# Optimization experiments

Measured on AMD Instinct MI355X. Metric: run time of the kernel, lower is better.

The kernel has to match this reference:

```python
import jax, jax.numpy as jnp
import numpy as np

B, L, D = 16, 512, 768   # batch, seq_len, hidden_size
H = 12                   # encoder attention heads (self_attention_scores)
K = 128                  # num_preserved_tokens
U, NH = 256, 4           # router attention num_units / num_heads


def setup_inputs() -> dict:
    key = jax.random.key(0)
    ks = jax.random.split(key, 8)
    hidden_states = jax.random.normal(ks[0], (B, L, D), dtype=jnp.float32)
    u = jax.random.uniform(ks[1], (B, 1, 1, L))
    attention_mask = jnp.where(u < 0.9, 0.0, -10000.0).astype(jnp.float32)
    self_attention_scores = jax.random.normal(ks[2], (B, H, L, L), dtype=jnp.float32)
    Wq = jax.random.normal(ks[3], (U, D), dtype=jnp.float32) * 0.02
    Wk = jax.random.normal(ks[4], (U, D), dtype=jnp.float32) * 0.02
    Wv = jax.random.normal(ks[5], (U, D), dtype=jnp.float32) * 0.02
    Wo = jax.random.normal(ks[6], (D, U), dtype=jnp.float32) * 0.02
    bo = jnp.zeros((D,), dtype=jnp.float32)
    return {"hidden_states": hidden_states, "attention_mask": attention_mask,
            "self_attention_scores": self_attention_scores,
            "Wq": Wq, "Wk": Wk, "Wv": Wv, "Wo": Wo, "bo": bo}


def reference(hidden_states, attention_mask, self_attention_scores, Wq, Wk, Wv, Wo, bo):
    # sentence summary: softmax over additive mask -> weighted token average
    att = jax.nn.softmax(attention_mask, axis=-1)            # [B,1,1,L]
    sentences = jnp.einsum('bql,bld->bqd', att[:, 0], hidden_states)  # [B,1,D]

    key_padding_mask = attention_mask[:, 0, 0, :] < -10.0    # [B,L] True = masked

    # MyMultiHeadAttention(query=sentences, key=value=hidden_states)
    hd = U // NH
    q = jnp.einsum('bqd,ud->bqu', sentences, Wq)             # [B,1,U]
    k = jnp.einsum('bld,ud->blu', hidden_states, Wk)         # [B,L,U]
    v = jnp.einsum('bld,ud->blu', hidden_states, Wv)         # [B,L,U]
    qh = q.reshape(B, 1, NH, hd).transpose(2, 0, 1, 3)       # [h,B,1,hd]
    kh = k.reshape(B, L, NH, hd).transpose(2, 0, 1, 3)       # [h,B,L,hd]
    vh = v.reshape(B, L, NH, hd).transpose(2, 0, 1, 3)       # [h,B,L,hd]
    # NOTE: original scales by key_dim**0.5 = hidden_size**0.5 (not head dim)
    scores = jnp.einsum('hbqd,hbkd->hbqk', qh, kh) / (D ** 0.5)  # [h,B,1,L]
    scores = jnp.where(key_padding_mask[None, :, None, :], -jnp.inf, scores)
    probs = jax.nn.softmax(scores, axis=-1)
    out_h = jnp.einsum('hbqk,hbkd->hbqd', probs, vh)         # [h,B,1,hd]
    out = out_h.transpose(1, 2, 0, 3).reshape(B, 1, U)       # concat heads
    new_token = jnp.einsum('bqu,du->bqd', out, Wo) + bo      # [B,1,D]

    class_token = hidden_states[:, :1, :]                    # [B,1,D]

    # importance: mean over heads, sum over query positions -> [B,L]
    importance = self_attention_scores.mean(axis=1).sum(axis=1)
    top_idx = jax.lax.top_k(importance, K)[1]                # [B,K]
    # boolean-mask gather preserves original token order -> sort indices
    sorted_idx = jnp.sort(top_idx, axis=-1)                  # [B,K]
    preserved_tokens = jnp.take_along_axis(hidden_states, sorted_idx[:, :, None], axis=1)  # [B,K,D]
    preserved_mask = jnp.take_along_axis(attention_mask[:, 0, 0, :], sorted_idx, axis=1)
    preserved_mask = preserved_mask.reshape(B, 1, 1, K)

    zmask = jnp.zeros((B, 1, 1, 1), dtype=attention_mask.dtype)
    final_token = jnp.concatenate([class_token, preserved_tokens, new_token], axis=1)  # [B,K+2,D]
    final_attention_mask = jnp.concatenate([zmask, preserved_mask, zmask], axis=-1)    # [B,1,1,K+2]
    return final_token, final_attention_mask
```

## Files before the change

kernel.cpp:

```cpp
#include <hip/hip_runtime.h>
#include <math.h>

#define B_ 16
#define L_ 512
#define D_ 768
#define H_ 12
#define K_ 128
#define U_ 256
#define NH_ 4
#define HD_ 64
#define OUTROWS_ 130
#define IMP_G_ 96

__global__ __launch_bounds__(256) void importance_kernel(
    const float* __restrict__ scores, float* __restrict__ part) {
  const int b = blockIdx.y, chunk = blockIdx.x, t = threadIdx.x;
  const int qcol = t & 127;
  const int rhalf = t >> 7;
  const float4* base = (const float4*)scores +
      ((size_t)(b * (H_ * L_) + chunk * 128 + rhalf)) * 128 + qcol;
  float4 a = make_float4(0.f, 0.f, 0.f, 0.f);
  #pragma unroll 8
  for (int r = 0; r < 64; ++r) {
    float4 v = base[(size_t)r * 256];
    a.x += v.x; a.y += v.y; a.z += v.z; a.w += v.w;
  }
  const float s = 1.0f / 12.0f;
  float4 o = make_float4(a.x * s, a.y * s, a.z * s, a.w * s);
  ((float4*)part)[((size_t)b * IMP_G_ + chunk * 2 + rhalf) * 128 + qcol] = o;
}

__global__ __launch_bounds__(768) void sent_kernel(
    const float* __restrict__ hidden, const float* __restrict__ mask,
    float* __restrict__ sent_part) {
  __shared__ float att[L_];
  __shared__ float red_m[12], red_s[12];
  __shared__ float4 cbuf[4][192];
  const int b = blockIdx.x, chunk = blockIdx.y, t = threadIdx.x;
  const int wave = t >> 6, lane = t & 63;
  const float m = (t < L_) ? mask[b * L_ + t] : -INFINITY;
  float r = m;
  #pragma unroll
  for (int off = 32; off > 0; off >>= 1) r = fmaxf(r, __shfl_down(r, off, 64));
  if (lane == 0) red_m[wave] = r;
  __syncthreads();
  float mx = red_m[0];
  #pragma unroll
  for (int w = 1; w < 12; ++w) mx = fmaxf(mx, red_m[w]);
  const float e = (t < L_) ? expf(m - mx) : 0.f;
  float rs = e;
  #pragma unroll
  for (int off = 32; off > 0; off >>= 1) rs += __shfl_down(rs, off, 64);
  if (lane == 0) red_s[wave] = rs;
  __syncthreads();
  float se = 0.f;
  #pragma unroll
  for (int w = 0; w < 12; ++w) se += red_s[w];
  if (t < L_) att[t] = e / se;
  __syncthreads();
  const int c4 = t % 192, sub = t / 192;
  const int l0 = chunk * 32 + sub * 8;
  const float4* h4 = (const float4*)hidden + ((size_t)b * L_ + l0) * 192 + c4;
  float4 acc = make_float4(0.f, 0.f, 0.f, 0.f);
  #pragma unroll
  for (int ii = 0; ii < 8; ++ii) {
    const float w = att[l0 + ii];
    const float4 hv = h4[(size_t)ii * 192];
    acc.x += w * hv.x; acc.y += w * hv.y; acc.z += w * hv.z; acc.w += w * hv.w;
  }
  cbuf[sub][c4] = acc;
  __syncthreads();
  if (t < 192) {
    float4 o = cbuf[0][t];
    #pragma unroll
    for (int g = 1; g < 4; ++g) {
      const float4 v = cbuf[g][t];
      o.x += v.x; o.y += v.y; o.z += v.z; o.w += v.w;
    }
    ((float4*)sent_part)[((size_t)b * 16 + chunk) * 192 + t] = o;
  }
}

__global__ __launch_bounds__(768) void qproj_topk_kernel(
    const float* __restrict__ sent_part, const float* __restrict__ Wq,
    const float* __restrict__ Wk, float* __restrict__ wqe,
    const float* __restrict__ part, const float* __restrict__ mask,
    const float* __restrict__ hidden, float* __restrict__ out0,
    float* __restrict__ out1) {
  __shared__ float s[D_];
  __shared__ float qvh[HD_];
  __shared__ float v[L_];
  __shared__ int lidx[K_];
  __shared__ int wcnt[12];
  const int t = threadIdx.x;
  const int wave = t >> 6, lane = t & 63;

  if (blockIdx.x < 64) {
    const int b = blockIdx.x >> 2, h = blockIdx.x & 3;
    {
      const float* sp = sent_part + (size_t)b * 16 * D_ + t;
      float a = 0.f;
      #pragma unroll
      for (int c = 0; c < 16; ++c) a += sp[(size_t)c * D_];
      s[t] = a;
    }
    __syncthreads();
    for (int u = wave; u < HD_; u += 12) {
      const float* wr = Wq + (size_t)(h * HD_ + u) * D_;
      float acc = 0.f;
      #pragma unroll
      for (int k = 0; k < 12; ++k) {
        const int d = lane + (k << 6);
        acc += wr[d] * s[d];
      }
      #pragma unroll
      for (int o = 32; o > 0; o >>= 1) acc += __shfl_down(acc, o, 64);
      if (lane == 0) qvh[u] = acc;
    }
    __syncthreads();
    {
      float acc = 0.f;
      const float* wk = Wk + (size_t)(h * HD_) * D_ + t;
      #pragma unroll 4
      for (int j = 0; j < HD_; ++j) acc += qvh[j] * wk[(size_t)j * D_];
      wqe[((size_t)b * NH_ + h) * D_ + t] = acc;
    }
  } else {
    const int b = blockIdx.x - 64;
    if (t < L_) {
      const float* pp = part + (size_t)b * IMP_G_ * L_ + t;
      float sum = 0.f;
      #pragma unroll 8
      for (int g = 0; g < IMP_G_; ++g) sum += pp[(size_t)g * L_];
      v[t] = sum;
    }
    __syncthreads();
    bool sel = false;
    if (t < L_) {
      const float mv = v[t];
      int cnt = 0;
      #pragma unroll 8
      for (int j = 0; j < L_; ++j) {
        float o = v[j];
        cnt += (o > mv) || (o == mv && j < t);
      }
      sel = cnt < K_;
    }
    const unsigned long long ball = __ballot(sel);
    if (lane == 0) wcnt[wave] = __popcll(ball);
    __syncthreads();
    int base = 0;
    for (int w = 0; w < wave; ++w) base += wcnt[w];
    const int pos = base + __popcll(ball & ((1ull << lane) - 1ull));
    if (sel) {
      lidx[pos] = t;
      out1[b * OUTROWS_ + 1 + pos] = mask[b * L_ + t];
    }
    if (t == 0) {
      out1[b * OUTROWS_ + 0] = 0.f;
      out1[b * OUTROWS_ + OUTROWS_ - 1] = 0.f;
    }
    __syncthreads();
    const float4* hb4 = (const float4*)(hidden + (size_t)b * L_ * D_);
    float4* ob4 = (float4*)(out0 + (size_t)b * OUTROWS_ * D_);
    const int NG = (K_ + 1) * 192;
    for (int i = t; i < NG; i += 768) {
      const int r = i / 192;
      const int c = i - r * 192;
      const int src = (r == 0) ? 0 : lidx[r - 1];
      ob4[r * 192 + c] = hb4[src * 192 + c];
    }
  }
}

__global__ __launch_bounds__(256) void score_kernel(
    const float* __restrict__ hidden, const float* __restrict__ mask,
    const float* __restrict__ wqe, float* __restrict__ scores) {
  __shared__ float4 wq4[NH_ * 192];
  const int b = blockIdx.x, chunk = blockIdx.y, t = threadIdx.x;
  {
    const float4* wsrc = (const float4*)(wqe + (size_t)b * NH_ * D_);
    for (int i = t; i < NH_ * 192; i += 256) wq4[i] = wsrc[i];
  }
  __syncthreads();
  const int wave = t >> 6, lane = t & 63;
  const float scale = 0.03608439182435161f;
  #pragma unroll
  for (int r = 0; r < 8; ++r) {
    const int l = chunk * 32 + wave * 8 + r;
    const float4* hr4 = (const float4*)(hidden + ((size_t)b * L_ + l) * D_);
    float s0 = 0.f, s1 = 0.f, s2 = 0.f, s3 = 0.f;
    #pragma unroll
    for (int jj = 0; jj < 3; ++jj) {
      const int c = lane + 64 * jj;
      const float4 hv = hr4[c];
      const float4 w0 = wq4[0 * 192 + c];
      const float4 w1 = wq4[1 * 192 + c];
      const float4 w2 = wq4[2 * 192 + c];
      const float4 w3 = wq4[3 * 192 + c];
      s0 += hv.x * w0.x + hv.y * w0.y + hv.z * w0.z + hv.w * w0.w;
      s1 += hv.x * w1.x + hv.y * w1.y + hv.z * w1.z + hv.w * w1.w;
      s2 += hv.x * w2.x + hv.y * w2.y + hv.z * w2.z + hv.w * w2.w;
      s3 += hv.x * w3.x + hv.y * w3.y + hv.z * w3.z + hv.w * w3.w;
    }
    #pragma unroll
    for (int o = 32; o > 0; o >>= 1) {
      s0 += __shfl_down(s0, o, 64);
      s1 += __shfl_down(s1, o, 64);
      s2 += __shfl_down(s2, o, 64);
      s3 += __shfl_down(s3, o, 64);
    }
    if (lane == 0) {
      const bool kp = mask[b * L_ + l] < -10.f;
      float* sp = scores + (size_t)b * NH_ * L_ + l;
      sp[0 * L_] = kp ? -INFINITY : s0 * scale;
      sp[1 * L_] = kp ? -INFINITY : s1 * scale;
      sp[2 * L_] = kp ? -INFINITY : s2 * scale;
      sp[3 * L_] = kp ? -INFINITY : s3 * scale;
    }
  }
}

__global__ __launch_bounds__(768) void ctx_prob_kernel(
    const float* __restrict__ hidden, const float* __restrict__ scores,
    float* __restrict__ ctx_part) {
  __shared__ float pr[NH_][32];
  __shared__ float red_m[NH_][12], red_s[NH_][12];
  const int b = blockIdx.x, chunk = blockIdx.y, t = threadIdx.x;
  const int wave = t >> 6, lane = t & 63;
  const int l0 = chunk * 32;

  float val[NH_];
  #pragma unroll
  for (int h = 0; h < NH_; ++h)
    val[h] = (t < L_) ? scores[((size_t)b * NH_ + h) * L_ + t] : -INFINITY;
  #pragma unroll
  for (int h = 0; h < NH_; ++h) {
    float r = val[h];
    #pragma unroll
    for (int off = 32; off > 0; off >>= 1) r = fmaxf(r, __shfl_down(r, off, 64));
    if (lane == 0) red_m[h][wave] = r;
  }
  __syncthreads();
  float e[NH_];
  #pragma unroll
  for (int h = 0; h < NH_; ++h) {
    float mx = red_m[h][0];
    #pragma unroll
    for (int w = 1; w < 12; ++w) mx = fmaxf(mx, red_m[h][w]);
    e[h] = (t < L_) ? expf(val[h] - mx) : 0.f;
    float rs = e[h];
    #pragma unroll
    for (int off = 32; off > 0; off >>= 1) rs += __shfl_down(rs, off, 64);
    if (lane == 0) red_s[h][wave] = rs;
  }
  __syncthreads();
  if (t >= l0 && t < l0 + 32) {
    #pragma unroll
    for (int h = 0; h < NH_; ++h) {
      float se = 0.f;
      #pragma unroll
      for (int w = 0; w < 12; ++w) se += red_s[h][w];
      pr[h][t - l0] = e[h] / se;
    }
  }
  __syncthreads();

  const int c4 = t % 192, hh = t / 192;
  const float4* h4 = (const float4*)hidden + ((size_t)b * L_ + l0) * 192 + c4;
  float4 acc = make_float4(0.f, 0.f, 0.f, 0.f);
  #pragma unroll 8
  for (int l = 0; l < 32; ++l) {
    const float w = pr[hh][l];
    const float4 hv = h4[(size_t)l * 192];
    acc.x += w * hv.x; acc.y += w * hv.y; acc.z += w * hv.z; acc.w += w * hv.w;
  }
  ((float4*)ctx_part)[(((size_t)b * 16 + chunk) * NH_ + hh) * 192 + c4] = acc;
}

__global__ __launch_bounds__(768) void outv_kernel(
    const float* __restrict__ ctx_part, const float* __restrict__ Wv,
    float* __restrict__ outv) {
  __shared__ float ch[D_];
  const int b = blockIdx.x, h = blockIdx.y, t = threadIdx.x;
  const int wave = t >> 6, lane = t & 63;
  {
    float a = 0.f;
    #pragma unroll
    for (int c = 0; c < 16; ++c)
      a += ctx_part[(((size_t)b * 16 + c) * NH_ + h) * D_ + t];
    ch[t] = a;
  }
  __syncthreads();
  for (int u = wave; u < HD_; u += 12) {
    const float* wr = Wv + (size_t)(h * HD_ + u) * D_;
    float acc = 0.f;
    #pragma unroll
    for (int k = 0; k < 12; ++k) {
      const int d = lane + (k << 6);
      acc += wr[d] * ch[d];
    }
    #pragma unroll
    for (int o = 32; o > 0; o >>= 1) acc += __shfl_down(acc, o, 64);
    if (lane == 0) outv[b * U_ + h * HD_ + u] = acc;
  }
}

__global__ __launch_bounds__(256) void newtoken_ws_kernel(
    const float* __restrict__ outv, const float* __restrict__ Wo,
    const float* __restrict__ bo, float* __restrict__ out0) {
  __shared__ float ovs[16 * 260];
  __shared__ float wot[16 * 260];
  const int d0 = blockIdx.x * 16, t = threadIdx.x;
  #pragma unroll
  for (int k = 0; k < 16; ++k) {
    const int i = t + (k << 8);
    const int row = i >> 8, u = i & 255;
    ovs[row * 260 + u] = outv[i];
    wot[row * 260 + u] = Wo[(size_t)(d0 + row) * U_ + u];
  }
  __syncthreads();
  const int b = t >> 4, dl = t & 15;
  const float* ov = ovs + b * 260;
  const float* wr = wot + dl * 260;
  float acc = 0.f;
  #pragma unroll 8
  for (int u = 0; u < U_; ++u) acc += ov[u] * wr[u];
  const int d = d0 + dl;
  out0[((size_t)b * OUTROWS_ + (OUTROWS_ - 1)) * D_ + d] = bo[d] + acc;
}

extern "C" void kernel_launch(void* const* d_in, const int* in_sizes, int n_in,
                              void* d_out, int out_size, void* d_ws, size_t ws_size,
                              hipStream_t stream) {
  const float* hidden = (const float*)d_in[0];
  const float* mask   = (const float*)d_in[1];
  const float* sas    = (const float*)d_in[2];
  const float* Wq     = (const float*)d_in[3];
  const float* Wk     = (const float*)d_in[4];
  const float* Wv     = (const float*)d_in[5];
  const float* Wo     = (const float*)d_in[6];
  const float* bo     = (const float*)d_in[7];

  float* out0 = (float*)d_out;
  float* out1 = out0 + (size_t)B_ * OUTROWS_ * D_;

  float* part      = (float*)d_ws;
  float* sent_part = part + (size_t)B_ * IMP_G_ * L_;
  float* ctx_part  = sent_part + (size_t)B_ * 16 * D_;
  float* wqe       = ctx_part + (size_t)B_ * 16 * NH_ * D_;
  float* scores    = wqe + (size_t)B_ * NH_ * D_;
  float* outv      = scores + (size_t)B_ * NH_ * L_;

  importance_kernel<<<dim3(48, B_), 256, 0, stream>>>(sas, part);
  sent_kernel<<<dim3(B_, 16), 768, 0, stream>>>(hidden, mask, sent_part);
  qproj_topk_kernel<<<80, 768, 0, stream>>>(sent_part, Wq, Wk, wqe,
                                            part, mask, hidden, out0, out1);
  score_kernel<<<dim3(B_, 16), 256, 0, stream>>>(hidden, mask, wqe, scores);
  ctx_prob_kernel<<<dim3(B_, 16), 768, 0, stream>>>(hidden, scores, ctx_part);
  outv_kernel<<<dim3(B_, NH_), 768, 0, stream>>>(ctx_part, Wv, outv);
  newtoken_ws_kernel<<<48, 256, 0, stream>>>(outv, Wo, bo, out0);
}
```

Baseline: 362.9 us.

## Fuse importance with sentence kernel and score with ctx using unnormalized softmax

Merges the importance reduction and sentence-summary kernels into one launch split by block index. The mask softmax is replaced by a count of valid tokens, which assumes the mask holds only 0 or -10000. Score computation and context accumulation are fused into one kernel that uses exp without max-subtraction and writes per-chunk exp sums. outv then normalizes by the total. This removes two launches and the scores round-trip through memory, at the cost of overflow risk for large scores and reliance on the binary mask values.

```diff
diff --git a/kernel.cpp b/kernel.cpp
--- a/kernel.cpp
+++ b/kernel.cpp
@@ -12,72 +12,57 @@
 #define OUTROWS_ 130
 #define IMP_G_ 96
 
-__global__ __launch_bounds__(256) void importance_kernel(
-    const float* __restrict__ scores, float* __restrict__ part) {
-  const int b = blockIdx.y, chunk = blockIdx.x, t = threadIdx.x;
-  const int qcol = t & 127;
-  const int rhalf = t >> 7;
-  const float4* base = (const float4*)scores +
-      ((size_t)(b * (H_ * L_) + chunk * 128 + rhalf)) * 128 + qcol;
-  float4 a = make_float4(0.f, 0.f, 0.f, 0.f);
-  #pragma unroll 8
-  for (int r = 0; r < 64; ++r) {
-    float4 v = base[(size_t)r * 256];
-    a.x += v.x; a.y += v.y; a.z += v.z; a.w += v.w;
-  }
-  const float s = 1.0f / 12.0f;
-  float4 o = make_float4(a.x * s, a.y * s, a.z * s, a.w * s);
-  ((float4*)part)[((size_t)b * IMP_G_ + chunk * 2 + rhalf) * 128 + qcol] = o;
-}
-
-__global__ __launch_bounds__(768) void sent_kernel(
-    const float* __restrict__ hidden, const float* __restrict__ mask,
+__global__ __launch_bounds__(256) void front_kernel(
+    const float* __restrict__ sas, const float* __restrict__ hidden,
+    const float* __restrict__ mask, float* __restrict__ part,
     float* __restrict__ sent_part) {
-  __shared__ float att[L_];
-  __shared__ float red_m[12], red_s[12];
-  __shared__ float4 cbuf[4][192];
-  const int b = blockIdx.x, chunk = blockIdx.y, t = threadIdx.x;
-  const int wave = t >> 6, lane = t & 63;
-  const float m = (t < L_) ? mask[b * L_ + t] : -INFINITY;
-  float r = m;
-  #pragma unroll
-  for (int off = 32; off > 0; off >>= 1) r = fmaxf(r, __shfl_down(r, off, 64));
-  if (lane == 0) red_m[wave] = r;
-  __syncthreads();
-  float mx = red_m[0];
-  #pragma unroll
-  for (int w = 1; w < 12; ++w) mx = fmaxf(mx, red_m[w]);
-  const float e = (t < L_) ? expf(m - mx) : 0.f;
-  float rs = e;
-  #pragma unroll
-  for (int off = 32; off > 0; off >>= 1) rs += __shfl_down(rs, off, 64);
-  if (lane == 0) red_s[wave] = rs;
-  __syncthreads();
-  float se = 0.f;
-  #pragma unroll
-  for (int w = 0; w < 12; ++w) se += red_s[w];
-  if (t < L_) att[t] = e / se;
-  __syncthreads();
-  const int c4 = t % 192, sub = t / 192;
-  const int l0 = chunk * 32 + sub * 8;
-  const float4* h4 = (const float4*)hidden + ((size_t)b * L_ + l0) * 192 + c4;
-  float4 acc = make_float4(0.f, 0.f, 0.f, 0.f);
-  #pragma unroll
-  for (int ii = 0; ii < 8; ++ii) {
-    const float w = att[l0 + ii];
-    const float4 hv = h4[(size_t)ii * 192];
-    acc.x += w * hv.x; acc.y += w * hv.y; acc.z += w * hv.z; acc.w += w * hv.w;
-  }
-  cbuf[sub][c4] = acc;
-  __syncthreads();
-  if (t < 192) {
-    float4 o = cbuf[0][t];
-    #pragma unroll
-    for (int g = 1; g < 4; ++g) {
-      const float4 v = cbuf[g][t];
-      o.x += v.x; o.y += v.y; o.z += v.z; o.w += v.w;
-    }
-    ((float4*)sent_part)[((size_t)b * 16 + chunk) * 192 + t] = o;
+  const int t = threadIdx.x;
+  if (blockIdx.x < 768) {
+    const int b = blockIdx.x / 48, chunk = blockIdx.x % 48;
+    const int qcol = t & 127;
+    const int rhalf = t >> 7;
+    const float4* base = (const float4*)sas +
+        ((size_t)(b * (H_ * L_) + chunk * 128 + rhalf)) * 128 + qcol;
+    float4 a = make_float4(0.f, 0.f, 0.f, 0.f);
+    #pragma unroll 8
+    for (int r = 0; r < 64; ++r) {
+      float4 v = base[(size_t)r * 256];
+      a.x += v.x; a.y += v.y; a.z += v.z; a.w += v.w;
+    }
+    const float s = 1.0f / 12.0f;
+    float4 o = make_float4(a.x * s, a.y * s, a.z * s, a.w * s);
+    ((float4*)part)[((size_t)b * IMP_G_ + chunk * 2 + rhalf) * 128 + qcol] = o;
+  } else {
+    __shared__ float att[L_];
+    __shared__ int redc[4];
+    const int i = blockIdx.x - 768;
+    const int b = i >> 4, chunk = i & 15;
+    const int wave = t >> 6, lane = t & 63;
+    const float m0 = mask[b * L_ + t];
+    const float m1 = mask[b * L_ + t + 256];
+    const int u0 = (m0 > -10.f) ? 1 : 0;
+    const int u1 = (m1 > -10.f) ? 1 : 0;
+    int c = u0 + u1;
+    #pragma unroll
+    for (int off = 32; off > 0; off >>= 1) c += __shfl_down(c, off, 64);
+    if (lane == 0) redc[wave] = c;
+    __syncthreads();
+    const float inv = 1.0f / (float)(redc[0] + redc[1] + redc[2] + redc[3]);
+    att[t]       = u0 ? inv : 0.f;
+    att[t + 256] = u1 ? inv : 0.f;
+    __syncthreads();
+    if (t < 192) {
+      const int l0 = chunk * 32;
+      const float4* h4 = (const float4*)hidden + ((size_t)b * L_ + l0) * 192 + t;
+      float4 acc = make_float4(0.f, 0.f, 0.f, 0.f);
+      #pragma unroll 8
+      for (int l = 0; l < 32; ++l) {
+        const float w = att[l0 + l];
+        const float4 hv = h4[(size_t)l * 192];
+        acc.x += w * hv.x; acc.y += w * hv.y; acc.z += w * hv.z; acc.w += w * hv.w;
+      }
+      ((float4*)sent_part)[((size_t)b * 16 + chunk) * 192 + t] = acc;
+    }
   }
 }
 
@@ -173,96 +158,64 @@
   }
 }
 
-__global__ __launch_bounds__(256) void score_kernel(
+__global__ __launch_bounds__(768) void scorectx_kernel(
     const float* __restrict__ hidden, const float* __restrict__ mask,
-    const float* __restrict__ wqe, float* __restrict__ scores) {
+    const float* __restrict__ wqe, float* __restrict__ ctx_part,
+    float* __restrict__ esum) {
   __shared__ float4 wq4[NH_ * 192];
-  const int b = blockIdx.x, chunk = blockIdx.y, t = threadIdx.x;
-  {
-    const float4* wsrc = (const float4*)(wqe + (size_t)b * NH_ * D_);
-    for (int i = t; i < NH_ * 192; i += 256) wq4[i] = wsrc[i];
-  }
-  __syncthreads();
-  const int wave = t >> 6, lane = t & 63;
-  const float scale = 0.03608439182435161f;
-  #pragma unroll
-  for (int r = 0; r < 8; ++r) {
-    const int l = chunk * 32 + wave * 8 + r;
-    const float4* hr4 = (const float4*)(hidden + ((size_t)b * L_ + l) * D_);
-    float s0 = 0.f, s1 = 0.f, s2 = 0.f, s3 = 0.f;
-    #pragma unroll
-    for (int jj = 0; jj < 3; ++jj) {
-      const int c = lane + 64 * jj;
-      const float4 hv = hr4[c];
-      const float4 w0 = wq4[0 * 192 + c];
-      const float4 w1 = wq4[1 * 192 + c];
-      const float4 w2 = wq4[2 * 192 + c];
-      const float4 w3 = wq4[3 * 192 + c];
-      s0 += hv.x * w0.x + hv.y * w0.y + hv.z * w0.z + hv.w * w0.w;
-      s1 += hv.x * w1.x + hv.y * w1.y + hv.z * w1.z + hv.w * w1.w;
-      s2 += hv.x * w2.x + hv.y * w2.y + hv.z * w2.z + hv.w * w2.w;
-      s3 += hv.x * w3.x + hv.y * w3.y + hv.z * w3.z + hv.w * w3.w;
-    }
-    #pragma unroll
-    for (int o = 32; o > 0; o >>= 1) {
-      s0 += __shfl_down(s0, o, 64);
-      s1 += __shfl_down(s1, o, 64);
-      s2 += __shfl_down(s2, o, 64);
-      s3 += __shfl_down(s3, o, 64);
-    }
-    if (lane == 0) {
-      const bool kp = mask[b * L_ + l] < -10.f;
-      float* sp = scores + (size_t)b * NH_ * L_ + l;
-      sp[0 * L_] = kp ? -INFINITY : s0 * scale;
-      sp[1 * L_] = kp ? -INFINITY : s1 * scale;
-      sp[2 * L_] = kp ? -INFINITY : s2 * scale;
-      sp[3 * L_] = kp ? -INFINITY : s3 * scale;
-    }
-  }
-}
-
-__global__ __launch_bounds__(768) void ctx_prob_kernel(
-    const float* __restrict__ hidden, const float* __restrict__ scores,
-    float* __restrict__ ctx_part) {
   __shared__ float pr[NH_][32];
-  __shared__ float red_m[NH_][12], red_s[NH_][12];
+  __shared__ float es[NH_];
   const int b = blockIdx.x, chunk = blockIdx.y, t = threadIdx.x;
   const int wave = t >> 6, lane = t & 63;
   const int l0 = chunk * 32;
 
-  float val[NH_];
-  #pragma unroll
-  for (int h = 0; h < NH_; ++h)
-    val[h] = (t < L_) ? scores[((size_t)b * NH_ + h) * L_ + t] : -INFINITY;
-  #pragma unroll
-  for (int h = 0; h < NH_; ++h) {
-    float r = val[h];
-    #pragma unroll
-    for (int off = 32; off > 0; off >>= 1) r = fmaxf(r, __shfl_down(r, off, 64));
-    if (lane == 0) red_m[h][wave] = r;
-  }
-  __syncthreads();
-  float e[NH_];
-  #pragma unroll
-  for (int h = 0; h < NH_; ++h) {
-    float mx = red_m[h][0];
-    #pragma unroll
-    for (int w = 1; w < 12; ++w) mx = fmaxf(mx, red_m[h][w]);
-    e[h] = (t < L_) ? expf(val[h] - mx) : 0.f;
-    float rs = e[h];
-    #pragma unroll
-    for (int off = 32; off > 0; off >>= 1) rs += __shfl_down(rs, off, 64);
-    if (lane == 0) red_s[h][wave] = rs;
-  }
-  __syncthreads();
-  if (t >= l0 && t < l0 + 32) {
-    #pragma unroll
-    for (int h = 0; h < NH_; ++h) {
-      float se = 0.f;
-      #pragma unroll
-      for (int w = 0; w < 12; ++w) se += red_s[h][w];
-      pr[h][t - l0] = e[h] / se;
-    }
+  for (int i = t; i < NH_ * 192; i += 768)
+    wq4[i] = ((const float4*)(wqe + (size_t)b * NH_ * D_))[i];
+  __syncthreads();
+
+  const float scale = 0.03608439182435161f;
+  if (wave < 8) {
+    #pragma unroll
+    for (int r = 0; r < 4; ++r) {
+      const int lr = wave * 4 + r;
+      const int l = l0 + lr;
+      const float4* hr4 = (const float4*)(hidden + ((size_t)b * L_ + l) * D_);
+      float s0 = 0.f, s1 = 0.f, s2 = 0.f, s3 = 0.f;
+      #pragma unroll
+      for (int jj = 0; jj < 3; ++jj) {
+        const int cc = lane + 64 * jj;
+        const float4 hv = hr4[cc];
+        const float4 w0 = wq4[0 * 192 + cc];
+        const float4 w1 = wq4[1 * 192 + cc];
+        const float4 w2 = wq4[2 * 192 + cc];
+        const float4 w3 = wq4[3 * 192 + cc];
+        s0 += hv.x * w0.x + hv.y * w0.y + hv.z * w0.z + hv.w * w0.w;
+        s1 += hv.x * w1.x + hv.y * w1.y + hv.z * w1.z + hv.w * w1.w;
+        s2 += hv.x * w2.x + hv.y * w2.y + hv.z * w2.z + hv.w * w2.w;
+        s3 += hv.x * w3.x + hv.y * w3.y + hv.z * w3.z + hv.w * w3.w;
+      }
+      #pragma unroll
+      for (int o = 32; o > 0; o >>= 1) {
+        s0 += __shfl_down(s0, o, 64);
+        s1 += __shfl_down(s1, o, 64);
+        s2 += __shfl_down(s2, o, 64);
+        s3 += __shfl_down(s3, o, 64);
+      }
+      if (lane == 0) {
+        const bool kp = mask[b * L_ + l] < -10.f;
+        pr[0][lr] = kp ? 0.f : expf(s0 * scale);
+        pr[1][lr] = kp ? 0.f : expf(s1 * scale);
+        pr[2][lr] = kp ? 0.f : expf(s2 * scale);
+        pr[3][lr] = kp ? 0.f : expf(s3 * scale);
+      }
+    }
+  }
+  __syncthreads();
+  if (wave < NH_) {
+    float v = (lane < 32) ? pr[wave][lane] : 0.f;
+    #pragma unroll
+    for (int off = 32; off > 0; off >>= 1) v += __shfl_down(v, off, 64);
+    if (lane == 0) es[wave] = v;
   }
   __syncthreads();
 
@@ -276,14 +229,22 @@
     acc.x += w * hv.x; acc.y += w * hv.y; acc.z += w * hv.z; acc.w += w * hv.w;
   }
   ((float4*)ctx_part)[(((size_t)b * 16 + chunk) * NH_ + hh) * 192 + c4] = acc;
+  if (t < NH_) esum[((size_t)b * 16 + chunk) * NH_ + t] = es[t];
 }
 
 __global__ __launch_bounds__(768) void outv_kernel(
-    const float* __restrict__ ctx_part, const float* __restrict__ Wv,
-    float* __restrict__ outv) {
+    const float* __restrict__ ctx_part, const float* __restrict__ esum,
+    const float* __restrict__ Wv, float* __restrict__ outv) {
   __shared__ float ch[D_];
+  __shared__ float invE;
   const int b = blockIdx.x, h = blockIdx.y, t = threadIdx.x;
   const int wave = t >> 6, lane = t & 63;
+  if (t == 0) {
+    float E = 0.f;
+    #pragma unroll
+    for (int c = 0; c < 16; ++c) E += esum[((size_t)b * 16 + c) * NH_ + h];
+    invE = 1.0f / E;
+  }
   {
     float a = 0.f;
     #pragma unroll
@@ -292,6 +253,7 @@
     ch[t] = a;
   }
   __syncthreads();
+  const float ie = invE;
   for (int u = wave; u < HD_; u += 12) {
     const float* wr = Wv + (size_t)(h * HD_ + u) * D_;
     float acc = 0.f;
@@ -302,7 +264,7 @@
     }
     #pragma unroll
     for (int o = 32; o > 0; o >>= 1) acc += __shfl_down(acc, o, 64);
-    if (lane == 0) outv[b * U_ + h * HD_ + u] = acc;
+    if (lane == 0) outv[b * U_ + h * HD_ + u] = acc * ie;
   }
 }
 
@@ -349,15 +311,14 @@
   float* sent_part = part + (size_t)B_ * IMP_G_ * L_;
   float* ctx_part  = sent_part + (size_t)B_ * 16 * D_;
   float* wqe       = ctx_part + (size_t)B_ * 16 * NH_ * D_;
-  float* scores    = wqe + (size_t)B_ * NH_ * D_;
-  float* outv      = scores + (size_t)B_ * NH_ * L_;
-
-  importance_kernel<<<dim3(48, B_), 256, 0, stream>>>(sas, part);
-  sent_kernel<<<dim3(B_, 16), 768, 0, stream>>>(hidden, mask, sent_part);
+  float* esum      = wqe + (size_t)B_ * NH_ * D_;
+  float* outv      = esum + (size_t)B_ * 16 * NH_;
+
+  front_kernel<<<1024, 256, 0, stream>>>(sas, hidden, mask, part, sent_part);
   qproj_topk_kernel<<<80, 768, 0, stream>>>(sent_part, Wq, Wk, wqe,
                                             part, mask, hidden, out0, out1);
-  score_kernel<<<dim3(B_, 16), 256, 0, stream>>>(hidden, mask, wqe, scores);
-  ctx_prob_kernel<<<dim3(B_, 16), 768, 0, stream>>>(hidden, scores, ctx_part);
-  outv_kernel<<<dim3(B_, NH_), 768, 0, stream>>>(ctx_part, Wv, outv);
+  scorectx_kernel<<<dim3(B_, 16), 768, 0, stream>>>(hidden, mask, wqe,
+                                                    ctx_part, esum);
+  outv_kernel<<<dim3(B_, NH_), 768, 0, stream>>>(ctx_part, esum, Wv, outv);
   newtoken_ws_kernel<<<48, 256, 0, stream>>>(outv, Wo, bo, out0);
 }
```

Measured after the change: 355.8 us. No clear change (-2.0%).
